# Kernel optimization log

Measured on AMD Instinct MI355X. Metric: run time of the kernel, lower is better.

## Reference

```python
import jax, jax.numpy as jnp
import numpy as np

B, S, D, H = 2, 2048, 1024, 16
HD = D // H  # 64

def setup_inputs() -> dict:
    key = jax.random.key(0)
    ks = jax.random.split(key, 6)
    s = 1.0 / np.sqrt(D)
    return {
        "x": jax.random.normal(ks[0], (B, S, D), dtype=jnp.float32),
        "wq": jax.random.normal(ks[1], (D, D), dtype=jnp.float32) * s,
        "wk": jax.random.normal(ks[2], (D, D), dtype=jnp.float32) * s,
        "wv": jax.random.normal(ks[3], (D, D), dtype=jnp.float32) * s,
        "wo": jax.random.normal(ks[4], (D, D), dtype=jnp.float32) * s,
        "bo": jax.random.normal(ks[5], (D,), dtype=jnp.float32) * 0.01,
    }

def reference(x, wq, wk, wv, wo, bo):
    b, s, _ = x.shape
    # QKV projections (qkvBias=False), reshape to [b, h, s, hd]
    q = (x @ wq).reshape(b, s, H, HD).transpose(0, 2, 1, 3)
    k = (x @ wk).reshape(b, s, H, HD).transpose(0, 2, 1, 3)
    v = (x @ wv).reshape(b, s, H, HD).transpose(0, 2, 1, 3)
    # scores, causal mask (upper triangle -> -inf), scale, softmax
    scores = jnp.einsum('bhqd,bhkd->bhqk', q, k)
    causal = jnp.triu(jnp.ones((s, s), dtype=bool), k=1)
    scores = jnp.where(causal, -jnp.inf, scores) / np.sqrt(HD)
    weights = jax.nn.softmax(scores, axis=-1)  # dropout=0 (eval)
    ctx = jnp.einsum('bhqk,bhkd->bhqd', weights, v)
    ctx = ctx.transpose(0, 2, 1, 3).reshape(b, s, D)
    return ctx @ wo + bo
```

## Files before the change

### kernel.cpp

```cpp
#include <hip/hip_runtime.h>
#include <hip/hip_bf16.h>
#include <math.h>

#define BB 2
#define SS 2048
#define DD 1024
#define HH 16
#define HDIM 64

typedef unsigned short u16;
typedef __attribute__((ext_vector_type(8))) short bfrag;
typedef __attribute__((ext_vector_type(4))) float f32x4;

#define NEG_BIG (-1e30f)
#define QSCALE 0.18033688011112042f

__device__ __forceinline__ u16 f2u(float f) {
    unsigned int u = __builtin_bit_cast(unsigned int, f);
    u += 0x7fffu + ((u >> 16) & 1u);
    return (u16)(u >> 16);
}

__device__ __forceinline__ void async16(const u16* g, u16* l) {
    __builtin_amdgcn_global_load_lds((__attribute__((address_space(1))) void*)g,
                                     (__attribute__((address_space(3))) void*)l,
                                     16, 0, 0);
}

__device__ __forceinline__ f32x4 mfma16(bfrag a, bfrag b, f32x4 c) {
    return __builtin_amdgcn_mfma_f32_16x16x32_bf16(a, b, c, 0, 0, 0);
}

__global__ __launch_bounds__(256) void prep_k(
    const float* __restrict__ x,  u16* __restrict__ xb,
    const float* __restrict__ wq, const float* __restrict__ wk,
    const float* __restrict__ wv, const float* __restrict__ wo,
    u16* __restrict__ wT)
{
    const int id = blockIdx.x;
    const int t = threadIdx.x;
    if (id < 2048) {
        int i = (id * 256 + t) * 8;
        float4 a = *(const float4*)(x + i);
        float4 b = *(const float4*)(x + i + 4);
        u16 o[8] = { f2u(a.x), f2u(a.y), f2u(a.z), f2u(a.w),
                     f2u(b.x), f2u(b.y), f2u(b.z), f2u(b.w) };
        *(uint4*)(xb + i) = *(uint4*)o;
        return;
    }
    const int wid = id - 2048;
    const int z = wid >> 8;
    const int kt = wid & 15, nt = (wid >> 4) & 15;
    const float* w = (z == 0) ? wq : (z == 1) ? wk : (z == 2) ? wv : wo;
    u16* o = wT + (size_t)z * DD * DD;
    __shared__ __align__(16) u16 T[64][72];
    const int k0 = kt * 64, n0 = nt * 64;
    {
        int kr = t >> 2, nb = (t & 3) * 16;
        const float4* s4 = (const float4*)(w + (size_t)(k0 + kr) * DD + n0 + nb);
        #pragma unroll
        for (int jj = 0; jj < 4; ++jj) {
            float4 v = s4[jj];
            T[kr][nb + jj*4 + 0] = f2u(v.x);
            T[kr][nb + jj*4 + 1] = f2u(v.y);
            T[kr][nb + jj*4 + 2] = f2u(v.z);
            T[kr][nb + jj*4 + 3] = f2u(v.w);
        }
    }
    __syncthreads();
    {
        int nr = t >> 2, kb = (t & 3) * 16;
        u16 tmp[16];
        #pragma unroll
        for (int j = 0; j < 16; ++j) tmp[j] = T[kb + j][nr];
        *(uint4*)(o + (size_t)(n0 + nr) * DD + k0 + kb)     = ((uint4*)tmp)[0];
        *(uint4*)(o + (size_t)(n0 + nr) * DD + k0 + kb + 8) = ((uint4*)tmp)[1];
    }
}

__global__ __launch_bounds__(256) void gemm_qkv_k(
    const u16* __restrict__ xb, const u16* __restrict__ wT,
    u16* __restrict__ Qo, u16* __restrict__ Ko, u16* __restrict__ Vt)
{
    const u16* wTz = wT + (size_t)blockIdx.z * DD * DD;
    const float osc = (blockIdx.z == 0) ? QSCALE : 1.0f;

    __shared__ __align__(16) u16 As[2][4096];
    __shared__ __align__(16) u16 Bs[2][4096];

    const int t = threadIdx.x;
    const int m0 = blockIdx.x * 128, n0 = blockIdx.y * 128;
    const int lane15 = t & 15, quad = (t >> 4) & 3, wave = t >> 6;
    const int wm = wave & 1, wn = wave >> 1;

    const int ar0 = t >> 2,        as0 = t & 3;
    const int ar1 = (t + 256) >> 2, as1 = (t + 256) & 3;
    const int ac0 = as0 ^ ((ar0 >> 1) & 3);
    const int ac1 = as1 ^ ((ar1 >> 1) & 3);
    const u16* gA0 = xb  + (size_t)(m0 + ar0) * DD + ac0 * 8;
    const u16* gA1 = xb  + (size_t)(m0 + ar1) * DD + ac1 * 8;
    const u16* gB0 = wTz + (size_t)(n0 + ar0) * DD + ac0 * 8;
    const u16* gB1 = wTz + (size_t)(n0 + ar1) * DD + ac1 * 8;
    const int ldst = (t & 192) * 8;

    int aoff[4], boff[4];
    #pragma unroll
    for (int mi = 0; mi < 4; ++mi) {
        int r = wm * 64 + mi * 16 + lane15;
        aoff[mi] = (r * 4 + (quad ^ ((r >> 1) & 3))) * 8;
    }
    #pragma unroll
    for (int ni = 0; ni < 4; ++ni) {
        int r = wn * 64 + ni * 16 + lane15;
        boff[ni] = (r * 4 + (quad ^ ((r >> 1) & 3))) * 8;
    }

    f32x4 acc[4][4];
    #pragma unroll
    for (int mi = 0; mi < 4; ++mi)
        #pragma unroll
        for (int ni = 0; ni < 4; ++ni)
            acc[mi][ni] = (f32x4){0.f, 0.f, 0.f, 0.f};

    async16(gA0, &As[0][ldst]);
    async16(gA1, &As[0][ldst + 2048]);
    async16(gB0, &Bs[0][ldst]);
    async16(gB1, &Bs[0][ldst + 2048]);

    for (int it = 0; it < 32; ++it) {
        __syncthreads();
        const int cb = it & 1, nb = cb ^ 1;
        if (it < 31) {
            const int nk = (it + 1) * 32;
            async16(gA0 + nk, &As[nb][ldst]);
            async16(gA1 + nk, &As[nb][ldst + 2048]);
            async16(gB0 + nk, &Bs[nb][ldst]);
            async16(gB1 + nk, &Bs[nb][ldst + 2048]);
        }
        bfrag av[4], bv[4];
        #pragma unroll
        for (int mi = 0; mi < 4; ++mi) av[mi] = *(const bfrag*)&As[cb][aoff[mi]];
        #pragma unroll
        for (int ni = 0; ni < 4; ++ni) bv[ni] = *(const bfrag*)&Bs[cb][boff[ni]];
        #pragma unroll
        for (int mi = 0; mi < 4; ++mi)
            #pragma unroll
            for (int ni = 0; ni < 4; ++ni)
                acc[mi][ni] = mfma16(av[mi], bv[ni], acc[mi][ni]);
    }

    if (blockIdx.z != 2) {
        u16* out = (blockIdx.z == 0) ? Qo : Ko;
        #pragma unroll
        for (int mi = 0; mi < 4; ++mi) {
            #pragma unroll
            for (int r = 0; r < 4; ++r) {
                int m = m0 + wm * 64 + mi * 16 + quad * 4 + r;
                int b = m >> 11, s = m & (SS - 1);
                #pragma unroll
                for (int ni = 0; ni < 4; ++ni) {
                    int n = n0 + wn * 64 + ni * 16 + lane15;
                    int h = n >> 6, hd = n & 63;
                    out[(((size_t)(b * HH + h)) * SS + s) * HDIM + hd] = f2u(acc[mi][ni][r] * osc);
                }
            }
        }
    } else {
        __syncthreads();
        u16* T = &As[0][0];
        const int bq = m0 >> 11;
        const int ms = m0 & (SS - 1);
        #pragma unroll
        for (int hh = 0; hh < 2; ++hh) {
            if (wn == hh) {
                #pragma unroll
                for (int mi = 0; mi < 4; ++mi)
                    #pragma unroll
                    for (int r = 0; r < 4; ++r) {
                        int ml = wm * 64 + mi * 16 + quad * 4 + r;
                        #pragma unroll
                        for (int ni = 0; ni < 4; ++ni) {
                            int nl = ni * 16 + lane15;
                            T[nl * 128 + (ml ^ ((nl & 7) << 4))] = f2u(acc[mi][ni][r]);
                        }
                    }
            }
            __syncthreads();
            const int h = (n0 >> 6) + hh;
            u16* dst = Vt + ((size_t)(bq * HH + h)) * (HDIM * SS);
            #pragma unroll
            for (int i = 0; i < 4; ++i) {
                int c = t + i * 256;
                int row = c >> 4;
                int mb  = (c & 15) * 8;
                uint4 val = *(const uint4*)&T[row * 128 + (mb ^ ((row & 7) << 4))];
                *(uint4*)(dst + (size_t)row * SS + ms + mb) = val;
            }
            __syncthreads();
        }
    }
}

__global__ __launch_bounds__(256) void gemm_out_k(
    const u16* __restrict__ ctxb, const u16* __restrict__ woT,
    const float* __restrict__ bo, float* __restrict__ out)
{
    __shared__ __align__(16) u16 As[2][4096];
    __shared__ __align__(16) u16 Bs[2][2048];

    const int t = threadIdx.x;
    const int m0 = blockIdx.x * 128, n0 = blockIdx.y * 64;
    const int lane15 = t & 15, quad = (t >> 4) & 3, wave = t >> 6;
    const int wm = wave & 1, wn = wave >> 1;

    const int ar0 = t >> 2,        as0 = t & 3;
    const int ar1 = (t + 256) >> 2, as1 = (t + 256) & 3;
    const int ac0 = as0 ^ ((ar0 >> 1) & 3);
    const int ac1 = as1 ^ ((ar1 >> 1) & 3);
    const u16* gA0 = ctxb + (size_t)(m0 + ar0) * DD + ac0 * 8;
    const u16* gA1 = ctxb + (size_t)(m0 + ar1) * DD + ac1 * 8;
    const u16* gB0 = woT  + (size_t)(n0 + ar0) * DD + ac0 * 8;
    const int ldst = (t & 192) * 8;

    int aoff[4], boff[2];
    #pragma unroll
    for (int mi = 0; mi < 4; ++mi) {
        int r = wm * 64 + mi * 16 + lane15;
        aoff[mi] = (r * 4 + (quad ^ ((r >> 1) & 3))) * 8;
    }
    #pragma unroll
    for (int ni = 0; ni < 2; ++ni) {
        int r = wn * 32 + ni * 16 + lane15;
        boff[ni] = (r * 4 + (quad ^ ((r >> 1) & 3))) * 8;
    }

    f32x4 acc[4][2];
    #pragma unroll
    for (int mi = 0; mi < 4; ++mi)
        #pragma unroll
        for (int ni = 0; ni < 2; ++ni)
            acc[mi][ni] = (f32x4){0.f, 0.f, 0.f, 0.f};

    async16(gA0, &As[0][ldst]);
    async16(gA1, &As[0][ldst + 2048]);
    async16(gB0, &Bs[0][ldst]);

    for (int it = 0; it < 32; ++it) {
        __syncthreads();
        const int cb = it & 1, nb = cb ^ 1;
        if (it < 31) {
            const int nk = (it + 1) * 32;
            async16(gA0 + nk, &As[nb][ldst]);
            async16(gA1 + nk, &As[nb][ldst + 2048]);
            async16(gB0 + nk, &Bs[nb][ldst]);
        }
        bfrag av[4], bv[2];
        #pragma unroll
        for (int mi = 0; mi < 4; ++mi) av[mi] = *(const bfrag*)&As[cb][aoff[mi]];
        #pragma unroll
        for (int ni = 0; ni < 2; ++ni) bv[ni] = *(const bfrag*)&Bs[cb][boff[ni]];
        #pragma unroll
        for (int mi = 0; mi < 4; ++mi)
            #pragma unroll
            for (int ni = 0; ni < 2; ++ni)
                acc[mi][ni] = mfma16(av[mi], bv[ni], acc[mi][ni]);
    }

    float bias[2];
    #pragma unroll
    for (int ni = 0; ni < 2; ++ni)
        bias[ni] = bo[n0 + wn * 32 + ni * 16 + lane15];

    #pragma unroll
    for (int mi = 0; mi < 4; ++mi) {
        #pragma unroll
        for (int r = 0; r < 4; ++r) {
            int m = m0 + wm * 64 + mi * 16 + quad * 4 + r;
            #pragma unroll
            for (int ni = 0; ni < 2; ++ni) {
                int n = n0 + wn * 32 + ni * 16 + lane15;
                out[(size_t)m * DD + n] = acc[mi][ni][r] + bias[ni];
            }
        }
    }
}

__global__ __launch_bounds__(256, 4) void attn_k(
    const u16* __restrict__ Q, const u16* __restrict__ K,
    const u16* __restrict__ Vt, u16* __restrict__ ctx)
{
    __shared__ __align__(16) u16 QP[64 * 64];
    __shared__ __align__(16) u16 Ks[2][64 * 64];
    __shared__ __align__(16) u16 Vs[2][64 * 64];

    const int t = threadIdx.x;
    const int lane15 = t & 15, quad = (t >> 4) & 3, wave = t >> 6;
    const int bh = blockIdx.x;
    const int qt = (int)(gridDim.y - 1) - (int)blockIdx.y;
    const int q0 = qt * 64;
    const int b = bh >> 4, h = bh & 15;

    const u16* Qb = Q  + (size_t)bh * SS * HDIM;
    const u16* Kb = K  + (size_t)bh * SS * HDIM;
    const u16* Vb = Vt + (size_t)bh * HDIM * SS;

    const int kr0 = t >> 3,         ks0 = t & 7;
    const int kr1 = (t + 256) >> 3, ks1 = (t + 256) & 7;
    const int kc0 = ks0 ^ (kr0 & 7);
    const int kc1 = ks1 ^ (kr1 & 7);
    const int ldst = (t & 192) * 8;

    async16(Qb + (size_t)(q0 + kr0) * HDIM + kc0 * 8, QP + ldst);
    async16(Qb + (size_t)(q0 + kr1) * HDIM + kc1 * 8, QP + ldst + 2048);
    async16(Kb + (size_t)kr0 * HDIM + kc0 * 8, &Ks[0][ldst]);
    async16(Kb + (size_t)kr1 * HDIM + kc1 * 8, &Ks[0][ldst + 2048]);
    async16(Vb + (size_t)kr0 * SS + kc0 * 8, &Vs[0][ldst]);
    async16(Vb + (size_t)kr1 * SS + kc1 * 8, &Vs[0][ldst + 2048]);

    const int qrow = wave * 16 + lane15;
    int qoff[2], koff[4][2];
    #pragma unroll
    for (int kh = 0; kh < 2; ++kh)
        qoff[kh] = (qrow * 8 + ((kh * 4 + quad) ^ (qrow & 7))) * 8;
    #pragma unroll
    for (int ni = 0; ni < 4; ++ni)
        #pragma unroll
        for (int kh = 0; kh < 2; ++kh) {
            int row = ni * 16 + lane15;
            koff[ni][kh] = (row * 8 + ((kh * 4 + quad) ^ (row & 7))) * 8;
        }

    __syncthreads();
    bfrag aq[2];
    aq[0] = *(const bfrag*)(QP + qoff[0]);
    aq[1] = *(const bfrag*)(QP + qoff[1]);
    __syncthreads();

    f32x4 acc_o[4];
    float rsum[4] = {0.f, 0.f, 0.f, 0.f};
    #pragma unroll
    for (int nd = 0; nd < 4; ++nd) acc_o[nd] = (f32x4){0.f, 0.f, 0.f, 0.f};

    const int qgb = q0 + wave * 16 + quad * 4;

    for (int kt = 0; kt <= qt; ++kt) {
        if (kt < qt) {
            const int nv0 = (kt + 1) * 64;
            const int pb = (kt + 1) & 1;
            async16(Kb + (size_t)(nv0 + kr0) * HDIM + kc0 * 8, &Ks[pb][ldst]);
            async16(Kb + (size_t)(nv0 + kr1) * HDIM + kc1 * 8, &Ks[pb][ldst + 2048]);
            async16(Vb + (size_t)kr0 * SS + nv0 + kc0 * 8, &Vs[pb][ldst]);
            async16(Vb + (size_t)kr1 * SS + nv0 + kc1 * 8, &Vs[pb][ldst + 2048]);
        }
        const int cb = kt & 1;
        const int kv0 = kt * 64;

        f32x4 s_acc[4];
        #pragma unroll
        for (int ni = 0; ni < 4; ++ni) s_acc[ni] = (f32x4){0.f, 0.f, 0.f, 0.f};
        #pragma unroll
        for (int kh = 0; kh < 2; ++kh)
            #pragma unroll
            for (int ni = 0; ni < 4; ++ni)
                s_acc[ni] = mfma16(aq[kh], *(const bfrag*)&Ks[cb][koff[ni][kh]], s_acc[ni]);

        const bool diag = (kt == qt);
        #pragma unroll
        for (int ni = 0; ni < 4; ++ni) {
            int kvg = kv0 + ni * 16 + lane15;
            #pragma unroll
            for (int r = 0; r < 4; ++r) {
                float v = s_acc[ni][r];
                if (diag && (kvg > qgb + r)) v = NEG_BIG;
                float pw = exp2f(v);
                unsigned pu = __builtin_bit_cast(unsigned, pw);
                rsum[r] += __builtin_bit_cast(float, pu & 0xffff0000u);
                int row = wave * 16 + quad * 4 + r;
                int col = ni * 16 + lane15;
                QP[(row * 8 + ((col >> 3) ^ (row & 7))) * 8 + (col & 7)] = (u16)(pu >> 16);
            }
        }

        #pragma unroll
        for (int kh = 0; kh < 2; ++kh) {
            bfrag ap = *(const bfrag*)(QP + qoff[kh]);
            #pragma unroll
            for (int nd = 0; nd < 4; ++nd)
                acc_o[nd] = mfma16(ap, *(const bfrag*)&Vs[cb][koff[nd][kh]], acc_o[nd]);
        }
        __syncthreads();
    }

    #pragma unroll
    for (int off = 1; off < 16; off <<= 1)
        #pragma unroll
        for (int r = 0; r < 4; ++r)
            rsum[r] += __shfl_xor(rsum[r], off, 64);

    #pragma unroll
    for (int r = 0; r < 4; ++r) {
        float inv = 1.f / rsum[r];
        int srow = q0 + wave * 16 + quad * 4 + r;
        size_t base = ((size_t)b * SS + srow) * DD + h * HDIM;
        #pragma unroll
        for (int nd = 0; nd < 4; ++nd)
            ctx[base + nd * 16 + lane15] = f2u(acc_o[nd][r] * inv);
    }
}

extern "C" void kernel_launch(void* const* d_in, const int* in_sizes, int n_in,
                              void* d_out, int out_size, void* d_ws, size_t ws_size,
                              hipStream_t stream) {
    const float* x  = (const float*)d_in[0];
    const float* wq = (const float*)d_in[1];
    const float* wk = (const float*)d_in[2];
    const float* wv = (const float*)d_in[3];
    const float* wo = (const float*)d_in[4];
    const float* bo = (const float*)d_in[5];
    float* out = (float*)d_out;

    char* ws = (char*)d_ws;
    const size_t MB8 = (size_t)8 * 1024 * 1024;
    u16* xb  = (u16*)(ws);
    u16* wT  = (u16*)(ws + MB8);
    u16* Qb  = (u16*)(ws + 2 * MB8);
    u16* Kb  = (u16*)(ws + 3 * MB8);
    u16* Vt  = (u16*)(ws + 4 * MB8);
    u16* ctxb = xb;

    prep_k  <<<3072, 256, 0, stream>>>(x, xb, wq, wk, wv, wo, wT);
    gemm_qkv_k<<<dim3(32, 8, 3), 256, 0, stream>>>(xb, wT, Qb, Kb, Vt);
    attn_k  <<<dim3(32, 32), 256, 0, stream>>>(Qb, Kb, Vt, ctxb);
    gemm_out_k<<<dim3(32, 16), 256, 0, stream>>>(ctxb, wT + (size_t)3 * DD * DD, bo, out);
}
```

Baseline: 195.4 us.

## Replace double-buffered K=32 GEMM loads with single-buffered K=64 tiles

After: 182.5 us. 1.07x faster.

```diff
diff --git a/kernel.cpp b/kernel.cpp
--- a/kernel.cpp
+++ b/kernel.cpp
@@ -85,34 +85,37 @@
     const u16* wTz = wT + (size_t)blockIdx.z * DD * DD;
     const float osc = (blockIdx.z == 0) ? QSCALE : 1.0f;
 
-    __shared__ __align__(16) u16 As[2][4096];
-    __shared__ __align__(16) u16 Bs[2][4096];
+    __shared__ __align__(16) u16 As[128 * 64];
+    __shared__ __align__(16) u16 Bs[128 * 64];
 
     const int t = threadIdx.x;
     const int m0 = blockIdx.x * 128, n0 = blockIdx.y * 128;
     const int lane15 = t & 15, quad = (t >> 4) & 3, wave = t >> 6;
     const int wm = wave & 1, wn = wave >> 1;
 
-    const int ar0 = t >> 2,        as0 = t & 3;
-    const int ar1 = (t + 256) >> 2, as1 = (t + 256) & 3;
-    const int ac0 = as0 ^ ((ar0 >> 1) & 3);
-    const int ac1 = as1 ^ ((ar1 >> 1) & 3);
-    const u16* gA0 = xb  + (size_t)(m0 + ar0) * DD + ac0 * 8;
-    const u16* gA1 = xb  + (size_t)(m0 + ar1) * DD + ac1 * 8;
-    const u16* gB0 = wTz + (size_t)(n0 + ar0) * DD + ac0 * 8;
-    const u16* gB1 = wTz + (size_t)(n0 + ar1) * DD + ac1 * 8;
-    const int ldst = (t & 192) * 8;
-
-    int aoff[4], boff[4];
+    int srow[4], scol[4];
+    #pragma unroll
+    for (int i = 0; i < 4; ++i) {
+        int c = t + i * 256;
+        srow[i] = c >> 3;
+        scol[i] = (c & 7) ^ (srow[i] & 7);
+    }
+    const int ldb = (t & 192) * 8;
+
+    int aoff[4][2], boff[4][2];
     #pragma unroll
     for (int mi = 0; mi < 4; ++mi) {
         int r = wm * 64 + mi * 16 + lane15;
-        aoff[mi] = (r * 4 + (quad ^ ((r >> 1) & 3))) * 8;
+        #pragma unroll
+        for (int kh = 0; kh < 2; ++kh)
+            aoff[mi][kh] = (r * 8 + ((kh * 4 + quad) ^ (r & 7))) * 8;
     }
     #pragma unroll
     for (int ni = 0; ni < 4; ++ni) {
         int r = wn * 64 + ni * 16 + lane15;
-        boff[ni] = (r * 4 + (quad ^ ((r >> 1) & 3))) * 8;
+        #pragma unroll
+        for (int kh = 0; kh < 2; ++kh)
+            boff[ni][kh] = (r * 8 + ((kh * 4 + quad) ^ (r & 7))) * 8;
     }
 
     f32x4 acc[4][4];
@@ -122,31 +125,30 @@
         for (int ni = 0; ni < 4; ++ni)
             acc[mi][ni] = (f32x4){0.f, 0.f, 0.f, 0.f};
 
-    async16(gA0, &As[0][ldst]);
-    async16(gA1, &As[0][ldst + 2048]);
-    async16(gB0, &Bs[0][ldst]);
-    async16(gB1, &Bs[0][ldst + 2048]);
-
-    for (int it = 0; it < 32; ++it) {
+    for (int it = 0; it < 16; ++it) {
+        const int k0 = it * 64;
+        #pragma unroll
+        for (int i = 0; i < 4; ++i) {
+            async16(xb  + (size_t)(m0 + srow[i]) * DD + k0 + scol[i] * 8,
+                    As + ldb + i * 2048);
+            async16(wTz + (size_t)(n0 + srow[i]) * DD + k0 + scol[i] * 8,
+                    Bs + ldb + i * 2048);
+        }
         __syncthreads();
-        const int cb = it & 1, nb = cb ^ 1;
-        if (it < 31) {
-            const int nk = (it + 1) * 32;
-            async16(gA0 + nk, &As[nb][ldst]);
-            async16(gA1 + nk, &As[nb][ldst + 2048]);
-            async16(gB0 + nk, &Bs[nb][ldst]);
-            async16(gB1 + nk, &Bs[nb][ldst + 2048]);
-        }
-        bfrag av[4], bv[4];
-        #pragma unroll
-        for (int mi = 0; mi < 4; ++mi) av[mi] = *(const bfrag*)&As[cb][aoff[mi]];
-        #pragma unroll
-        for (int ni = 0; ni < 4; ++ni) bv[ni] = *(const bfrag*)&Bs[cb][boff[ni]];
-        #pragma unroll
-        for (int mi = 0; mi < 4; ++mi)
-            #pragma unroll
-            for (int ni = 0; ni < 4; ++ni)
-                acc[mi][ni] = mfma16(av[mi], bv[ni], acc[mi][ni]);
+        #pragma unroll
+        for (int kh = 0; kh < 2; ++kh) {
+            bfrag av[4], bv[4];
+            #pragma unroll
+            for (int mi = 0; mi < 4; ++mi) av[mi] = *(const bfrag*)(As + aoff[mi][kh]);
+            #pragma unroll
+            for (int ni = 0; ni < 4; ++ni) bv[ni] = *(const bfrag*)(Bs + boff[ni][kh]);
+            #pragma unroll
+            for (int mi = 0; mi < 4; ++mi)
+                #pragma unroll
+                for (int ni = 0; ni < 4; ++ni)
+                    acc[mi][ni] = mfma16(av[mi], bv[ni], acc[mi][ni]);
+        }
+        __syncthreads();
     }
 
     if (blockIdx.z != 2) {
@@ -166,8 +168,7 @@
             }
         }
     } else {
-        __syncthreads();
-        u16* T = &As[0][0];
+        u16* T = As;
         const int bq = m0 >> 11;
         const int ms = m0 & (SS - 1);
         #pragma unroll
@@ -205,33 +206,37 @@
     const u16* __restrict__ ctxb, const u16* __restrict__ woT,
     const float* __restrict__ bo, float* __restrict__ out)
 {
-    __shared__ __align__(16) u16 As[2][4096];
-    __shared__ __align__(16) u16 Bs[2][2048];
+    __shared__ __align__(16) u16 As[128 * 64];
+    __shared__ __align__(16) u16 Bs[64 * 64];
 
     const int t = threadIdx.x;
     const int m0 = blockIdx.x * 128, n0 = blockIdx.y * 64;
     const int lane15 = t & 15, quad = (t >> 4) & 3, wave = t >> 6;
     const int wm = wave & 1, wn = wave >> 1;
 
-    const int ar0 = t >> 2,        as0 = t & 3;
-    const int ar1 = (t + 256) >> 2, as1 = (t + 256) & 3;
-    const int ac0 = as0 ^ ((ar0 >> 1) & 3);
-    const int ac1 = as1 ^ ((ar1 >> 1) & 3);
-    const u16* gA0 = ctxb + (size_t)(m0 + ar0) * DD + ac0 * 8;
-    const u16* gA1 = ctxb + (size_t)(m0 + ar1) * DD + ac1 * 8;
-    const u16* gB0 = woT  + (size_t)(n0 + ar0) * DD + ac0 * 8;
-    const int ldst = (t & 192) * 8;
-
-    int aoff[4], boff[2];
+    int srow[4], scol[4];
+    #pragma unroll
+    for (int i = 0; i < 4; ++i) {
+        int c = t + i * 256;
+        srow[i] = c >> 3;
+        scol[i] = (c & 7) ^ (srow[i] & 7);
+    }
+    const int ldb = (t & 192) * 8;
+
+    int aoff[4][2], boff[2][2];
     #pragma unroll
     for (int mi = 0; mi < 4; ++mi) {
         int r = wm * 64 + mi * 16 + lane15;
-        aoff[mi] = (r * 4 + (quad ^ ((r >> 1) & 3))) * 8;
+        #pragma unroll
+        for (int kh = 0; kh < 2; ++kh)
+            aoff[mi][kh] = (r * 8 + ((kh * 4 + quad) ^ (r & 7))) * 8;
     }
     #pragma unroll
     for (int ni = 0; ni < 2; ++ni) {
         int r = wn * 32 + ni * 16 + lane15;
-        boff[ni] = (r * 4 + (quad ^ ((r >> 1) & 3))) * 8;
+        #pragma unroll
+        for (int kh = 0; kh < 2; ++kh)
+            boff[ni][kh] = (r * 8 + ((kh * 4 + quad) ^ (r & 7))) * 8;
     }
 
     f32x4 acc[4][2];
@@ -241,29 +246,31 @@
         for (int ni = 0; ni < 2; ++ni)
             acc[mi][ni] = (f32x4){0.f, 0.f, 0.f, 0.f};
 
-    async16(gA0, &As[0][ldst]);
-    async16(gA1, &As[0][ldst + 2048]);
-    async16(gB0, &Bs[0][ldst]);
-
-    for (int it = 0; it < 32; ++it) {
+    for (int it = 0; it < 16; ++it) {
+        const int k0 = it * 64;
+        #pragma unroll
+        for (int i = 0; i < 4; ++i)
+            async16(ctxb + (size_t)(m0 + srow[i]) * DD + k0 + scol[i] * 8,
+                    As + ldb + i * 2048);
+        #pragma unroll
+        for (int i = 0; i < 2; ++i)
+            async16(woT + (size_t)(n0 + srow[i]) * DD + k0 + scol[i] * 8,
+                    Bs + ldb + i * 2048);
         __syncthreads();
-        const int cb = it & 1, nb = cb ^ 1;
-        if (it < 31) {
-            const int nk = (it + 1) * 32;
-            async16(gA0 + nk, &As[nb][ldst]);
-            async16(gA1 + nk, &As[nb][ldst + 2048]);
-            async16(gB0 + nk, &Bs[nb][ldst]);
-        }
-        bfrag av[4], bv[2];
-        #pragma unroll
-        for (int mi = 0; mi < 4; ++mi) av[mi] = *(const bfrag*)&As[cb][aoff[mi]];
-        #pragma unroll
-        for (int ni = 0; ni < 2; ++ni) bv[ni] = *(const bfrag*)&Bs[cb][boff[ni]];
-        #pragma unroll
-        for (int mi = 0; mi < 4; ++mi)
-            #pragma unroll
-            for (int ni = 0; ni < 2; ++ni)
-                acc[mi][ni] = mfma16(av[mi], bv[ni], acc[mi][ni]);
+        #pragma unroll
+        for (int kh = 0; kh < 2; ++kh) {
+            bfrag av[4], bv[2];
+            #pragma unroll
+            for (int mi = 0; mi < 4; ++mi) av[mi] = *(const bfrag*)(As + aoff[mi][kh]);
+            #pragma unroll
+            for (int ni = 0; ni < 2; ++ni) bv[ni] = *(const bfrag*)(Bs + boff[ni][kh]);
+            #pragma unroll
+            for (int mi = 0; mi < 4; ++mi)
+                #pragma unroll
+                for (int ni = 0; ni < 2; ++ni)
+                    acc[mi][ni] = mfma16(av[mi], bv[ni], acc[mi][ni]);
+        }
+        __syncthreads();
     }
 
     float bias[2];
```
